# Kernel tuning notes

Hardware: AMD Instinct MI355X
Metric: run time of the kernel (lower is better)

Reference implementation:

```python
import jax, jax.numpy as jnp
import numpy as np

MAX_DEPTH = 8          # inner-node depths 1..8; leaves at depth 9
LMBDA = 0.1            # args.lmbda; per-node lmbda = LMBDA * 2**(-depth)
EPS = 1e-6


def setup_inputs() -> dict:
    key = jax.random.key(0)
    ks = jax.random.split(key, 7)
    B, D, O = 16384, 2048, 1000
    n_inner = 2 ** MAX_DEPTH - 1   # 255
    n_leaf = 2 ** MAX_DEPTH       # 256
    x = jax.random.normal(ks[0], (B, D), dtype=jnp.float32)
    target = jax.random.randint(ks[1], (B,), 0, O)
    y = jax.nn.one_hot(target, O, dtype=jnp.float32)  # target_onehot
    W = jax.random.normal(ks[2], (n_inner, D), dtype=jnp.float32) / np.sqrt(D)
    b = jax.random.normal(ks[3], (n_inner,), dtype=jnp.float32) * 0.01
    beta = jax.random.normal(ks[4], (n_inner,), dtype=jnp.float32)
    leaf_params = jax.random.normal(ks[5], (n_leaf, O), dtype=jnp.float32)
    return {"x": x, "y": y, "W": W, "b": b, "beta": beta, "leaf_params": leaf_params}


def reference(x, y, W, b, beta, leaf_params):
    """Faithful vectorized version of SoftDecisionTree.cal_loss.
    Inner nodes are stored in level-order (heap) layout, left-to-right
    within each level, matching the left-first recursion of cal_prob.
    Returns (loss, output) like cal_loss.
    """
    B = x.shape[0]
    dt = x.dtype
    # All inner-node gates in one fused GEMM: sigmoid(beta * (x @ w + b))
    probs = jax.nn.sigmoid(beta * (x @ W.T + b))  # [B, n_inner]

    path = jnp.ones((B, 1), dt)  # path_prob_init
    C = jnp.asarray(0.0, dt)
    idx = 0
    for d in range(1, MAX_DEPTH + 1):  # small fixed loop over tree levels
        n = 2 ** (d - 1)
        p = probs[:, idx:idx + n]      # gate probs for this level's nodes [B, n]
        if d < MAX_DEPTH:              # get_penalty skips nodes whose children are leaves
            denom = jnp.sum(path, axis=0)                  # [n]
            denom = jnp.where(denom == 0, EPS, denom)
            alpha = jnp.sum(p * path, axis=0) / denom      # [n]
            alpha = jnp.clip(alpha, EPS, 1.0 - EPS)
            lmbda = LMBDA * 2.0 ** (-d)
            C = C - jnp.sum(lmbda * 0.5 * (jnp.log(alpha) + jnp.log1p(-alpha)))
        # children: left gets path*(1-p), right gets path*p, interleaved
        path = jnp.stack([path * (1.0 - p), path * p], axis=-1).reshape(B, 2 * n)
        idx += n
    # path: [B, n_leaf] leaf arrival probabilities (left-to-right leaf order)

    logQ = jax.nn.log_softmax(leaf_params, axis=-1)  # [n_leaf, O]
    TQ = y @ logQ.T                                  # [B, n_leaf]: y . log Q per leaf
    loss_term = jnp.mean(jnp.sum(path * TQ, axis=1))
    loss = -loss_term + C

    best = jnp.argmax(path, axis=1)   # first max, matches the '<' update order
    output = jnp.exp(logQ)[best]      # [B, O] max_Q
    return loss, output
```

## Files before the change

kernel.cpp:

```cpp
#include <hip/hip_runtime.h>


typedef __attribute__((ext_vector_type(8))) short short8;
typedef __attribute__((ext_vector_type(4))) float f32x4;

#define DIM 2048
#define NCLS 1000
#define NINNER 255
#define NPAD 256
#define BM 32

__device__ __forceinline__ unsigned cvt2bf(float a, float b) {
  return ((__float_as_uint(a) + 0x8000u) >> 16) | ((__float_as_uint(b) + 0x8000u) & 0xFFFF0000u);
}

__global__ __launch_bounds__(256) void prep_w(const float* __restrict__ W,
                                              const float* __restrict__ b,
                                              const float* __restrict__ beta,
                                              unsigned short* __restrict__ WbP,
                                              float* __restrict__ bp,
                                              float* __restrict__ betap) {
  int f = blockIdx.x * 256 + threadIdx.x;
  int kt = f >> 10;
  int T = (f >> 6) & 15;
  int l = f & 63;
  int row = T * 16 + (l & 15);
  int k0 = kt * 32 + (l >> 4) * 8;
  uint4 o = make_uint4(0u, 0u, 0u, 0u);
  if (row < NINNER) {
    const float* src = W + (size_t)row * DIM + k0;
    o.x = cvt2bf(src[0], src[1]);
    o.y = cvt2bf(src[2], src[3]);
    o.z = cvt2bf(src[4], src[5]);
    o.w = cvt2bf(src[6], src[7]);
  }
  *(uint4*)(WbP + (size_t)f * 8) = o;
  if (f < NPAD) {
    bp[f] = (f < NINNER) ? b[f] : 0.f;
    betap[f] = (f < NINNER) ? beta[f] : 0.f;
  }
}

__global__ __launch_bounds__(256) void leaf_softmax(const float* __restrict__ leaf,
                                                    float* __restrict__ logQT,
                                                    float* __restrict__ Q) {
  int l = blockIdx.x, t = threadIdx.x;
  const float* row = leaf + (size_t)l * NCLS;
  __shared__ float red[256];
  float mx = -3.4e38f;
  for (int j = t; j < NCLS; j += 256) mx = fmaxf(mx, row[j]);
  red[t] = mx; __syncthreads();
  for (int s = 128; s; s >>= 1) { if (t < s) red[t] = fmaxf(red[t], red[t + s]); __syncthreads(); }
  mx = red[0]; __syncthreads();
  float sm = 0.f;
  for (int j = t; j < NCLS; j += 256) sm += __expf(row[j] - mx);
  red[t] = sm; __syncthreads();
  for (int s = 128; s; s >>= 1) { if (t < s) red[t] += red[t + s]; __syncthreads(); }
  float lse = mx + __logf(red[0]);
  for (int j = t; j < NCLS; j += 256) {
    float lg = row[j] - lse;
    logQT[(size_t)j * NPAD + l] = lg;
    Q[(size_t)l * NCLS + j] = __expf(lg);
  }
}

__global__ __launch_bounds__(256) void find_targets(const float* __restrict__ y,
                                                    int* __restrict__ tgt) {
  int wv = threadIdx.x >> 6, lane = threadIdx.x & 63;
  int r = blockIdx.x * 4 + wv;
  const float4* yr = (const float4*)(y + (size_t)r * NCLS);
  int found = 0x7fffffff;
#pragma unroll
  for (int i = 0; i < 4; ++i) {
    int j4 = i * 64 + lane;
    if (j4 < 250) {
      float4 v = yr[j4];
      if (v.x > 0.5f) found = min(found, 4 * j4 + 0);
      if (v.y > 0.5f) found = min(found, 4 * j4 + 1);
      if (v.z > 0.5f) found = min(found, 4 * j4 + 2);
      if (v.w > 0.5f) found = min(found, 4 * j4 + 3);
    }
  }
  for (int off = 32; off; off >>= 1) found = min(found, __shfl_down(found, off));
  if (lane == 0) tgt[r] = found;
}

#define DECLF(S) float4 S##a00, S##a01, S##a10, S##a11; short8 S##b0, S##b1, S##b2, S##b3;

#define LOADK(S, kt) do {                                                    \
  const float* _a0 = arow0 + (size_t)(kt) * 32;                              \
  const float* _a1 = arow1 + (size_t)(kt) * 32;                              \
  S##a00 = *(const float4*)_a0;  S##a01 = *(const float4*)(_a0 + 4);         \
  S##a10 = *(const float4*)_a1;  S##a11 = *(const float4*)(_a1 + 4);         \
  const unsigned short* _b = bptr + (size_t)(kt) * 8192;                     \
  S##b0 = *(const short8*)(_b);        S##b1 = *(const short8*)(_b + 512);   \
  S##b2 = *(const short8*)(_b + 1024); S##b3 = *(const short8*)(_b + 1536);  \
} while (0)

#define COMPUTE(S, AC) do {                                                  \
  short8 _afr0, _afr1;                                                       \
  { union { uint4 u; short8 s; } cv;                                         \
    cv.u.x = cvt2bf(S##a00.x, S##a00.y); cv.u.y = cvt2bf(S##a00.z, S##a00.w);\
    cv.u.z = cvt2bf(S##a01.x, S##a01.y); cv.u.w = cvt2bf(S##a01.z, S##a01.w);\
    _afr0 = cv.s; }                                                          \
  { union { uint4 u; short8 s; } cv;                                         \
    cv.u.x = cvt2bf(S##a10.x, S##a10.y); cv.u.y = cvt2bf(S##a10.z, S##a10.w);\
    cv.u.z = cvt2bf(S##a11.x, S##a11.y); cv.u.w = cvt2bf(S##a11.z, S##a11.w);\
    _afr1 = cv.s; }                                                          \
  AC[0][0] = __builtin_amdgcn_mfma_f32_16x16x32_bf16(_afr0, S##b0, AC[0][0], 0, 0, 0); \
  AC[1][0] = __builtin_amdgcn_mfma_f32_16x16x32_bf16(_afr1, S##b0, AC[1][0], 0, 0, 0); \
  AC[0][1] = __builtin_amdgcn_mfma_f32_16x16x32_bf16(_afr0, S##b1, AC[0][1], 0, 0, 0); \
  AC[1][1] = __builtin_amdgcn_mfma_f32_16x16x32_bf16(_afr1, S##b1, AC[1][1], 0, 0, 0); \
  AC[0][2] = __builtin_amdgcn_mfma_f32_16x16x32_bf16(_afr0, S##b2, AC[0][2], 0, 0, 0); \
  AC[1][2] = __builtin_amdgcn_mfma_f32_16x16x32_bf16(_afr1, S##b2, AC[1][2], 0, 0, 0); \
  AC[0][3] = __builtin_amdgcn_mfma_f32_16x16x32_bf16(_afr0, S##b3, AC[0][3], 0, 0, 0); \
  AC[1][3] = __builtin_amdgcn_mfma_f32_16x16x32_bf16(_afr1, S##b3, AC[1][3], 0, 0, 0); \
} while (0)

__global__ __launch_bounds__(256, 2) void gemm_tree(
    const float* __restrict__ x, const unsigned short* __restrict__ WbP,
    const float* __restrict__ bp, const float* __restrict__ betap,
    const float* __restrict__ logQT, const int* __restrict__ tgt,
    float* __restrict__ acc, int* __restrict__ best) {
  __shared__ __align__(16) float Ps[32 * 256];
  __shared__ float s0s[127], s1s[127], sdot;

  int tid = threadIdx.x;
  int lane = tid & 63, wave = tid >> 6;
  int frow = lane & 15, fq = lane >> 4;
  int m_base = blockIdx.x * BM;

  if (tid < 127) { s0s[tid] = 0.f; s1s[tid] = 0.f; }
  if (tid == 255) sdot = 0.f;

  const float* arow0 = x + (size_t)(m_base + frow) * DIM + fq * 8;
  const float* arow1 = arow0 + (size_t)16 * DIM;
  const unsigned short* bptr = WbP + ((size_t)wave * 256 + lane) * 8;

  f32x4 accA[2][4] = {}, accB[2][4] = {};

  DECLF(s0_) DECLF(s1_) DECLF(s2_) DECLF(s3_)
  LOADK(s0_, 0); LOADK(s1_, 1); LOADK(s2_, 2);

  for (int kt = 0; kt < 32; kt += 4) {
    LOADK(s3_, kt + 3);
    COMPUTE(s0_, accA); LOADK(s0_, kt + 4);
    COMPUTE(s1_, accA); LOADK(s1_, kt + 5);
    COMPUTE(s2_, accA); LOADK(s2_, kt + 6);
    COMPUTE(s3_, accA);
  }
  for (int kt = 32; kt < 64; kt += 4) {
    LOADK(s3_, kt + 3);
    COMPUTE(s0_, accB); if (kt < 60) LOADK(s0_, kt + 4);
    COMPUTE(s1_, accB); if (kt < 60) LOADK(s1_, kt + 5);
    COMPUTE(s2_, accB); if (kt < 60) LOADK(s2_, kt + 6);
    COMPUTE(s3_, accB);
  }

  __syncthreads();

#pragma unroll
  for (int mt = 0; mt < 2; ++mt)
#pragma unroll
    for (int nt = 0; nt < 4; ++nt)
#pragma unroll
      for (int rg = 0; rg < 4; ++rg)
        Ps[(mt * 16 + fq * 4 + rg) * 256 + wave * 64 + nt * 16 + frow] =
            accA[mt][nt][rg] + accB[mt][nt][rg];
  __syncthreads();

  {
    float bc2 = bp[tid], bec = betap[tid];
#pragma unroll 4
    for (int i = 0; i < 32; ++i) {
      float v = Ps[i * 256 + tid];
      Ps[i * 256 + tid] = 1.f / (1.f + __expf(-bec * (v + bc2)));
    }
  }
  __syncthreads();

  float wdot = 0.f;
  float s0r[7] = {}, s1r[7] = {};
  for (int it = 0; it < 8; ++it) {
    int rl = wave * 8 + it;
    int r = m_base + rl;
    const float* wsp = Ps + rl * 256;
    int tg = tgt[r];
    float pp = 1.f;
#pragma unroll
    for (int d = 1; d <= 6; ++d) {
      int idx = (1 << (d - 1)) - 1 + (lane >> (7 - d));
      float p = wsp[idx];
      s0r[d - 1] += pp;
      s1r[d - 1] += p * pp;
      pp *= ((lane >> (6 - d)) & 1) ? p : (1.f - p);
    }
    float p7 = wsp[63 + lane];
    s0r[6] += pp;
    s1r[6] += p7 * pp;
    float pL = pp * (1.f - p7), pR = pp * p7;
    float p8a = wsp[127 + 2 * lane], p8b = wsp[128 + 2 * lane];
    float lf0 = pL * (1.f - p8a), lf1 = pL * p8a;
    float lf2 = pR * (1.f - p8b), lf3 = pR * p8b;
    float4 lq = *(const float4*)(logQT + (size_t)tg * NPAD + lane * 4);
    wdot += lf0 * lq.x + lf1 * lq.y + lf2 * lq.z + lf3 * lq.w;
    float bv = lf0; int bi = 4 * lane;
    if (lf1 > bv) { bv = lf1; bi = 4 * lane + 1; }
    if (lf2 > bv) { bv = lf2; bi = 4 * lane + 2; }
    if (lf3 > bv) { bv = lf3; bi = 4 * lane + 3; }
    for (int off = 32; off; off >>= 1) {
      float ov = __shfl_down(bv, off);
      int oi = __shfl_down(bi, off);
      if (ov > bv || (ov == bv && oi < bi)) { bv = ov; bi = oi; }
    }
    if (lane == 0) best[r] = bi;
  }
#pragma unroll
  for (int d = 1; d <= 6; ++d) {
    int idx = (1 << (d - 1)) - 1 + (lane >> (7 - d));
    if ((lane & ((1 << (7 - d)) - 1)) == 0) {
      atomicAdd(&s0s[idx], s0r[d - 1]);
      atomicAdd(&s1s[idx], s1r[d - 1]);
    }
  }
  atomicAdd(&s0s[63 + lane], s0r[6]);
  atomicAdd(&s1s[63 + lane], s1r[6]);
  for (int off = 32; off; off >>= 1) wdot += __shfl_down(wdot, off);
  if (lane == 0) atomicAdd(&sdot, wdot);
  __syncthreads();
  if (tid < 127) {
    atomicAdd(&acc[tid], s0s[tid]);
    atomicAdd(&acc[127 + tid], s1s[tid]);
  }
  if (tid == 255) atomicAdd(&acc[254], sdot);
}

__global__ __launch_bounds__(128) void finalize_loss(const float* __restrict__ acc,
                                                     float* __restrict__ out) {
  __shared__ float red[128];
  int t = threadIdx.x;
  float c = 0.f;
  if (t < 127) {
    float denom = acc[t];
    if (denom == 0.f) denom = 1e-6f;
    float alpha = acc[127 + t] / denom;
    alpha = fminf(fmaxf(alpha, 1e-6f), 1.f - 1e-6f);
    int d = 31 - __clz(t + 1) + 1;
    float lm = 0.1f * exp2f(-(float)d);
    c = -lm * 0.5f * (logf(alpha) + log1pf(-alpha));
  }
  red[t] = c;
  __syncthreads();
  for (int s = 64; s; s >>= 1) { if (t < s) red[t] += red[t + s]; __syncthreads(); }
  if (t == 0) out[0] = -(acc[254] / 16384.f) + red[0];
}

__global__ __launch_bounds__(256) void gather_rows(const float* __restrict__ Q,
                                                   const int* __restrict__ best,
                                                   float* __restrict__ out) {
  int wv = threadIdx.x >> 6, lane = threadIdx.x & 63;
  int r = blockIdx.x * 4 + wv;
  const float* src = Q + (size_t)best[r] * NCLS;
  float* dst = out + 1 + (size_t)r * NCLS;
  if (lane < 3) dst[lane] = src[lane];
  if (lane == 0) dst[999] = src[999];
#pragma unroll
  for (int i = 0; i < 4; ++i) {
    int q = i * 64 + lane;
    if (q < 249) {
      int o = 3 + 4 * q;
      float4 v = make_float4(src[o], src[o + 1], src[o + 2], src[o + 3]);
      *(float4*)(dst + o) = v;
    }
  }
}

extern "C" void kernel_launch(void* const* d_in, const int* in_sizes, int n_in,
                              void* d_out, int out_size, void* d_ws, size_t ws_size,
                              hipStream_t stream) {
  const float* x = (const float*)d_in[0];
  const float* y = (const float*)d_in[1];
  const float* W = (const float*)d_in[2];
  const float* b = (const float*)d_in[3];
  const float* beta = (const float*)d_in[4];
  const float* leaf = (const float*)d_in[5];
  float* out = (float*)d_out;
  char* ws = (char*)d_ws;

  unsigned short* WbP = (unsigned short*)(ws + 0);
  float* bp    = (float*)(ws + 1048576);
  float* betap = (float*)(ws + 1049600);
  float* accb  = (float*)(ws + 1050624);
  int* tgt     = (int*)(ws + 1051648);
  int* best    = (int*)(ws + 1117184);
  float* logQT = (float*)(ws + 1182720);
  float* Q     = (float*)(ws + 2206720);

  prep_w<<<256, 256, 0, stream>>>(W, b, beta, WbP, bp, betap);
  leaf_softmax<<<256, 256, 0, stream>>>(leaf, logQT, Q);
  find_targets<<<4096, 256, 0, stream>>>(y, tgt);
  hipMemsetAsync(accb, 0, 256 * sizeof(float), stream);
  gemm_tree<<<512, 256, 0, stream>>>(x, WbP, bp, betap, logQT, tgt, accb, best);
  finalize_loss<<<1, 128, 0, stream>>>(accb, out);
  gather_rows<<<4096, 256, 0, stream>>>(Q, best, out);
}
```

Measured before the change: 339.8 us.

## Split GEMM N dimension across eight waves with shallower load pipeline

Doubles the block to 512 threads so each of eight waves computes 32 gate columns instead of 64. The register-prefetch pipeline drops from four stages to two, which shrinks per-thread register state and targets higher occupancy to hide memory latency. The sigmoid pass and the per-row tree pass are redistributed so each wave handles 16 rows and 4 rows respectively. In exchange, every wave now loads the same x rows, doubling x fetch traffic per block, and the shallower prefetch exposes more load latency per wave.

```diff
diff --git a/kernel.cpp b/kernel.cpp
--- a/kernel.cpp
+++ b/kernel.cpp
@@ -85,7 +85,7 @@
   if (lane == 0) tgt[r] = found;
 }
 
-#define DECLF(S) float4 S##a00, S##a01, S##a10, S##a11; short8 S##b0, S##b1, S##b2, S##b3;
+#define DECLF(S) float4 S##a00, S##a01, S##a10, S##a11; short8 S##b0, S##b1;
 
 #define LOADK(S, kt) do {                                                    \
   const float* _a0 = arow0 + (size_t)(kt) * 32;                              \
@@ -93,8 +93,7 @@
   S##a00 = *(const float4*)_a0;  S##a01 = *(const float4*)(_a0 + 4);         \
   S##a10 = *(const float4*)_a1;  S##a11 = *(const float4*)(_a1 + 4);         \
   const unsigned short* _b = bptr + (size_t)(kt) * 8192;                     \
-  S##b0 = *(const short8*)(_b);        S##b1 = *(const short8*)(_b + 512);   \
-  S##b2 = *(const short8*)(_b + 1024); S##b3 = *(const short8*)(_b + 1536);  \
+  S##b0 = *(const short8*)(_b);  S##b1 = *(const short8*)(_b + 512);         \
 } while (0)
 
 #define COMPUTE(S, AC) do {                                                  \
@@ -111,13 +110,9 @@
   AC[1][0] = __builtin_amdgcn_mfma_f32_16x16x32_bf16(_afr1, S##b0, AC[1][0], 0, 0, 0); \
   AC[0][1] = __builtin_amdgcn_mfma_f32_16x16x32_bf16(_afr0, S##b1, AC[0][1], 0, 0, 0); \
   AC[1][1] = __builtin_amdgcn_mfma_f32_16x16x32_bf16(_afr1, S##b1, AC[1][1], 0, 0, 0); \
-  AC[0][2] = __builtin_amdgcn_mfma_f32_16x16x32_bf16(_afr0, S##b2, AC[0][2], 0, 0, 0); \
-  AC[1][2] = __builtin_amdgcn_mfma_f32_16x16x32_bf16(_afr1, S##b2, AC[1][2], 0, 0, 0); \
-  AC[0][3] = __builtin_amdgcn_mfma_f32_16x16x32_bf16(_afr0, S##b3, AC[0][3], 0, 0, 0); \
-  AC[1][3] = __builtin_amdgcn_mfma_f32_16x16x32_bf16(_afr1, S##b3, AC[1][3], 0, 0, 0); \
 } while (0)
 
-__global__ __launch_bounds__(256, 2) void gemm_tree(
+__global__ __launch_bounds__(512, 4) void gemm_tree(
     const float* __restrict__ x, const unsigned short* __restrict__ WbP,
     const float* __restrict__ bp, const float* __restrict__ betap,
     const float* __restrict__ logQT, const int* __restrict__ tgt,
@@ -135,26 +130,24 @@
 
   const float* arow0 = x + (size_t)(m_base + frow) * DIM + fq * 8;
   const float* arow1 = arow0 + (size_t)16 * DIM;
-  const unsigned short* bptr = WbP + ((size_t)wave * 256 + lane) * 8;
-
-  f32x4 accA[2][4] = {}, accB[2][4] = {};
-
-  DECLF(s0_) DECLF(s1_) DECLF(s2_) DECLF(s3_)
-  LOADK(s0_, 0); LOADK(s1_, 1); LOADK(s2_, 2);
-
-  for (int kt = 0; kt < 32; kt += 4) {
-    LOADK(s3_, kt + 3);
-    COMPUTE(s0_, accA); LOADK(s0_, kt + 4);
-    COMPUTE(s1_, accA); LOADK(s1_, kt + 5);
-    COMPUTE(s2_, accA); LOADK(s2_, kt + 6);
-    COMPUTE(s3_, accA);
-  }
-  for (int kt = 32; kt < 64; kt += 4) {
-    LOADK(s3_, kt + 3);
-    COMPUTE(s0_, accB); if (kt < 60) LOADK(s0_, kt + 4);
-    COMPUTE(s1_, accB); if (kt < 60) LOADK(s1_, kt + 5);
-    COMPUTE(s2_, accB); if (kt < 60) LOADK(s2_, kt + 6);
-    COMPUTE(s3_, accB);
+  const unsigned short* bptr = WbP + ((size_t)wave * 2 * 64 + lane) * 8;
+
+  f32x4 accA[2][2] = {}, accB[2][2] = {};
+
+  DECLF(s0_) DECLF(s1_)
+  LOADK(s0_, 0);
+
+  for (int kt = 0; kt < 32; kt += 2) {
+    LOADK(s1_, kt + 1);
+    COMPUTE(s0_, accA);
+    LOADK(s0_, kt + 2);
+    COMPUTE(s1_, accA);
+  }
+  for (int kt = 32; kt < 64; kt += 2) {
+    LOADK(s1_, kt + 1);
+    COMPUTE(s0_, accB);
+    if (kt < 62) LOADK(s0_, kt + 2);
+    COMPUTE(s1_, accB);
   }
 
   __syncthreads();
@@ -162,27 +155,29 @@
 #pragma unroll
   for (int mt = 0; mt < 2; ++mt)
 #pragma unroll
-    for (int nt = 0; nt < 4; ++nt)
+    for (int nt = 0; nt < 2; ++nt)
 #pragma unroll
       for (int rg = 0; rg < 4; ++rg)
-        Ps[(mt * 16 + fq * 4 + rg) * 256 + wave * 64 + nt * 16 + frow] =
+        Ps[(mt * 16 + fq * 4 + rg) * 256 + wave * 32 + nt * 16 + frow] =
             accA[mt][nt][rg] + accB[mt][nt][rg];
   __syncthreads();
 
   {
-    float bc2 = bp[tid], bec = betap[tid];
+    int col = tid & 255;
+    int r0 = (tid >> 8) * 16;
+    float bc2 = bp[col], bec = betap[col];
 #pragma unroll 4
-    for (int i = 0; i < 32; ++i) {
-      float v = Ps[i * 256 + tid];
-      Ps[i * 256 + tid] = 1.f / (1.f + __expf(-bec * (v + bc2)));
+    for (int i = r0; i < r0 + 16; ++i) {
+      float v = Ps[i * 256 + col];
+      Ps[i * 256 + col] = 1.f / (1.f + __expf(-bec * (v + bc2)));
     }
   }
   __syncthreads();
 
   float wdot = 0.f;
   float s0r[7] = {}, s1r[7] = {};
-  for (int it = 0; it < 8; ++it) {
-    int rl = wave * 8 + it;
+  for (int it = 0; it < 4; ++it) {
+    int rl = wave * 4 + it;
     int r = m_base + rl;
     const float* wsp = Ps + rl * 256;
     int tg = tgt[r];
@@ -300,7 +295,7 @@
   leaf_softmax<<<256, 256, 0, stream>>>(leaf, logQT, Q);
   find_targets<<<4096, 256, 0, stream>>>(y, tgt);
   hipMemsetAsync(accb, 0, 256 * sizeof(float), stream);
-  gemm_tree<<<512, 256, 0, stream>>>(x, WbP, bp, betap, logQT, tgt, accb, best);
+  gemm_tree<<<512, 512, 0, stream>>>(x, WbP, bp, betap, logQT, tgt, accb, best);
   finalize_loss<<<1, 128, 0, stream>>>(accb, out);
   gather_rows<<<4096, 256, 0, stream>>>(Q, best, out);
 }
```

After: 386.4 us. +13.7%, slower.
